# Optimization experiments

Measured on AMD Instinct MI355X. Metric: run time of the kernel, lower is better.

Reference implementation:

```python
import jax, jax.numpy as jnp
from jax import lax
import numpy as np

DN = ('NDHWC', 'DHWIO', 'NDHWC')

def _conv(x, W):
    # stride-1 kernel-3 sparse conv on dense grid: SAME conv; absent voxels are zero
    return lax.conv_general_dilated(x, W, (1, 1, 1), 'SAME', dimension_numbers=DN)

def _tconv(x, W):
    # kernel-2 stride-2 generative transpose conv: exactly doubles each spatial dim
    return lax.conv_transpose(x, W, (2, 2, 2), 'VALID', dimension_numbers=DN)

def _pool(h):
    B, D1, D2, D3, C = h.shape
    return h.reshape(B, D1 // 2, 2, D2 // 2, 2, D3 // 2, 2, C).max(axis=(2, 4, 6))

def _pool_mask(m):
    B, D1, D2, D3 = m.shape
    return m.reshape(B, D1 // 2, 2, D2 // 2, 2, D3 // 2, 2).max(axis=(2, 4, 6))

def _up_mask(m):
    return jnp.repeat(jnp.repeat(jnp.repeat(m, 2, axis=1), 2, axis=2), 2, axis=3)

def setup_inputs() -> dict:
    key = jax.random.key(0)
    ks = jax.random.split(key, 6)
    B, G = 2, 128
    x = jax.random.normal(ks[0], (B, G, G, G, 1), dtype=jnp.float32)
    occ = jax.random.randint(ks[1], (B, G, G, G), 0, 10, dtype=jnp.int32)
    def xavier(k, shape):
        fan_in = np.prod(shape[:-1]); fan_out = shape[-1]
        std = np.sqrt(2.0 / (fan_in + fan_out)).astype(np.float32)
        return jax.random.normal(k, shape, dtype=jnp.float32) * std
    W1 = xavier(ks[2], (3, 3, 3, 1, 16))
    W2 = xavier(ks[3], (3, 3, 3, 16, 4))
    Wt1 = xavier(ks[4], (2, 2, 2, 4, 16))
    Wt2 = xavier(ks[5], (2, 2, 2, 16, 1))
    return {"x": x, "W1": W1, "W2": W2, "Wt1": Wt1, "Wt2": Wt2, "occ": occ}

def reference(x, W1, W2, Wt1, Wt2, occ):
    m0 = (occ == 0).astype(x.dtype)            # occupancy mask at full res
    xm = x * m0[..., None]
    h = jax.nn.relu(_conv(xm, W1)) * m0[..., None]   # coords unchanged
    h = _pool(h); m1 = _pool_mask(m0)                # stride-2 max pool on sparse coords
    h = jax.nn.relu(_conv(h, W2)) * m1[..., None]
    h = _pool(h); m2 = _pool_mask(m1)
    m3 = _up_mask(m2)                                # transpose conv emits all children coords
    h = jax.nn.relu(_tconv(h, Wt1)) * m3[..., None]
    m4 = _up_mask(m3)
    out = jax.nn.sigmoid(_tconv(h, Wt2)) * m4[..., None]
    return out
```

## Files before the change

### kernel.cpp

```cpp
#include <hip/hip_runtime.h>
#include <hip/hip_fp16.h>

#define G 128

typedef _Float16 h2_t __attribute__((ext_vector_type(2)));

union U16 { uint4 u; h2_t h2[4]; };
union HV  { uint4 u; h2_t h2[4]; };
union PK2 { uint2 u; h2_t h[2]; };

__device__ __forceinline__ float dot2f(h2_t a, h2_t b, float c) {
#if __has_builtin(__builtin_amdgcn_fdot2)
    return __builtin_amdgcn_fdot2(a, b, c, false);
#else
    return c + (float)a.x * (float)b.x + (float)a.y * (float)b.y;
#endif
}

__device__ __forceinline__ float dot4(float4 a, float4 b) {
    return a.x * b.x + a.y * b.y + a.z * b.z + a.w * b.w;
}

__global__ __launch_bounds__(256, 1)
void k_conv1_pool(const float* __restrict__ x, const int* __restrict__ occ,
                  const float* __restrict__ W1,
                  __half* __restrict__ h1p, float* __restrict__ m1)
{
    __shared__ __align__(16) _Float16      sx[10 * 18 * 24];
    __shared__ __align__(16) int           pacc[16 * 256];
    __shared__ __align__(4)  unsigned short slist[2048];
    __shared__ __align__(16) h2_t          w1L[216];
    __shared__ __align__(4)  unsigned char sm1[256];
    __shared__ int                         scnt;

    const int bx = blockIdx.x, by = blockIdx.y;
    const int b  = blockIdx.z >> 4, zt = blockIdx.z & 15;
    const int tid = threadIdx.x;

    const int z0 = zt * 8 - 1, y0 = by * 16 - 1;
    const int base_b = b * G * G * G;

    int4   ro[5];
    float4 rx[5];
    #pragma unroll
    for (int it = 0; it < 5; ++it) {
        int c = it * 256 + tid;
        int cc = c < 1080 ? c : 1079;
        int row = cc / 6, seg = cc - row * 6;
        int lz  = row / 18, ly = row - lz * 18;
        int gz = z0 + lz, gy = y0 + ly;
        int gxc = (bx << 4) - 4 + (seg << 2);
        bool inb = (unsigned)gz < 128u && (unsigned)gy < 128u && (unsigned)gxc < 128u;
        int gi = inb ? base_b + (gz * G + gy) * G + gxc : base_b;
        ro[it] = *(const int4*)(occ + gi);
        rx[it] = *(const float4*)(x + gi);
    }

    if (tid == 0) scnt = 0;
    {
        uint4 z4 = make_uint4(0u, 0u, 0u, 0u);
        uint4* p4 = (uint4*)pacc;
        p4[tid] = z4; p4[tid + 256] = z4; p4[tid + 512] = z4; p4[tid + 768] = z4;
    }
    if (tid < 64) ((unsigned*)sm1)[tid] = 0u;
    if (tid < 216) {
        float2 f = ((const float2*)W1)[tid];
        h2_t w; w.x = (_Float16)f.x; w.y = (_Float16)f.y;
        w1L[tid] = w;
    }
    __syncthreads();

    #pragma unroll
    for (int it = 0; it < 5; ++it) {
        int c = it * 256 + tid;
        if (c < 1080) {
            int row = c / 6, seg = c - row * 6;
            int lz  = row / 18, ly = row - lz * 18;
            int gz = z0 + lz, gy = y0 + ly;
            int gxc = (bx << 4) - 4 + (seg << 2);
            bool inb = (unsigned)gz < 128u && (unsigned)gy < 128u && (unsigned)gxc < 128u;
            int4   o4 = ro[it];
            float4 x4 = rx[it];
            if (!inb) o4 = make_int4(1, 1, 1, 1);
            h2_t p01, p23;
            p01.x = (o4.x == 0) ? (_Float16)x4.x : (_Float16)0.f;
            p01.y = (o4.y == 0) ? (_Float16)x4.y : (_Float16)0.f;
            p23.x = (o4.z == 0) ? (_Float16)x4.z : (_Float16)0.f;
            p23.y = (o4.w == 0) ? (_Float16)x4.w : (_Float16)0.f;
            PK2 pk; pk.h[0] = p01; pk.h[1] = p23;
            *(uint2*)&sx[row * 24 + (seg << 2)] = pk.u;

            if ((unsigned)(lz - 1) < 8u && (unsigned)(ly - 1) < 16u &&
                (unsigned)(seg - 1) < 4u) {
                int mb = (o4.x == 0 ? 1 : 0) | (o4.y == 0 ? 2 : 0) |
                         (o4.z == 0 ? 4 : 0) | (o4.w == 0 ? 8 : 0);
                if (mb) {
                    int cnt  = __popc(mb);
                    int base = atomicAdd(&scnt, cnt);
                    int cz = lz - 1, cy = ly - 1, cx0v = (seg << 2) - 4;
                    int cellb = (cz >> 1) * 64 + (cy >> 1) * 8;
                    #pragma unroll
                    for (int j = 0; j < 4; ++j) {
                        if (mb & (1 << j)) {
                            slist[base++] = (unsigned short)((cz << 8) | (cy << 4) | (cx0v + j));
                            sm1[cellb + ((cx0v + j) >> 1)] = (unsigned char)1;
                        }
                    }
                }
            }
        }
    }
    __syncthreads();

    const int n = scnt;

    const h2_t zero = (h2_t)(_Float16)0.f;
    for (int kb = 0; kb < n; kb += 256) {
        const int idx = kb + tid;
        if (idx < n) {
            const int code = slist[idx];
            const int cz = code >> 8, cy = (code >> 4) & 15, cx = code & 15;
            const int sb = ((cz + 1) * 18 + (cy + 1)) * 24 + cx + 4;
            h2_t acc[8];
            #pragma unroll
            for (int c = 0; c < 8; ++c) acc[c] = zero;
            #pragma unroll
            for (int kz = 0; kz < 3; ++kz)
            #pragma unroll
            for (int ky = 0; ky < 3; ++ky)
            #pragma unroll
            for (int kx = 0; kx < 3; ++kx) {
                _Float16 v = sx[sb + (kz - 1) * 432 + (ky - 1) * 24 + (kx - 1)];
                h2_t v2 = {v, v};
                const h2_t* w = &w1L[((kz * 3 + ky) * 3 + kx) * 8];
                #pragma unroll
                for (int c = 0; c < 8; ++c) acc[c] = v2 * w[c] + acc[c];
            }
            const int cell = (cz >> 1) * 64 + (cy >> 1) * 8 + (cx >> 1);
            #pragma unroll
            for (int c = 0; c < 8; ++c) {
                atomicMax(&pacc[(2 * c) * 256 + cell],
                          __float_as_int(fmaxf((float)acc[c].x, 0.f)));
                atomicMax(&pacc[(2 * c + 1) * 256 + cell],
                          __float_as_int(fmaxf((float)acc[c].y, 0.f)));
            }
        }
    }
    __syncthreads();

    const int tx = tid & 7, ty = (tid >> 3) & 7, tz = tid >> 6;
    const int pz = zt * 4 + tz, py = by * 8 + ty, px = bx * 8 + tx;
    const int vidx = ((b * 64 + pz) * 64 + py) * 64 + px;
    HV p0, p1;
    #pragma unroll
    for (int c = 0; c < 4; ++c) {
        h2_t a, bq;
        a.x  = (_Float16)__int_as_float(pacc[(2 * c) * 256 + tid]);
        a.y  = (_Float16)__int_as_float(pacc[(2 * c + 1) * 256 + tid]);
        bq.x = (_Float16)__int_as_float(pacc[(8 + 2 * c) * 256 + tid]);
        bq.y = (_Float16)__int_as_float(pacc[(9 + 2 * c) * 256 + tid]);
        p0.h2[c] = a; p1.h2[c] = bq;
    }
    uint4* o = (uint4*)&h1p[(size_t)vidx * 16];
    o[0] = p0.u;
    o[1] = p1.u;
    m1[vidx] = sm1[tid] ? 1.f : 0.f;
}

__global__ __launch_bounds__(256)
void k_conv2_dec(const __half* __restrict__ h1p, const float* __restrict__ m1,
                 const float* __restrict__ W2,
                 const float* __restrict__ Wt1, const float* __restrict__ Wt2,
                 float* __restrict__ out)
{
    __shared__ uint4  tile[2200];
    __shared__ float4 wt1[128];
    __shared__ float4 wt2[32];
    __shared__ __align__(16) h2_t w2L[864];
    __shared__ float4 sh_h[64];
    __shared__ float  sh_m[64];

    const int bx = blockIdx.x, by = blockIdx.y;
    const int b  = blockIdx.z >> 3, bz = blockIdx.z & 7;
    const int tid = threadIdx.x;

    const int z0 = bz * 8 - 1, y0 = by * 8 - 1, x0 = bx * 8 - 1;

    uint4 ra[5], rb4[5];
    #pragma unroll
    for (int it = 0; it < 5; ++it) {
        int g = it * 256 + tid;
        int gg = g < 1100 ? g : 1099;
        int z = gg / 110, r = gg - z * 110, y = r / 11, xx = r - y * 11;
        int gz = z0 + z, gy = y0 + y, gx = x0 + xx;
        bool inb = (unsigned)gz < 64u && (unsigned)gy < 64u && (unsigned)gx < 64u;
        size_t vi = inb ? (size_t)(((b * 64 + gz) * 64 + gy) * 64 + gx) : 0;
        const uint4* src = (const uint4*)&h1p[vi * 16];
        ra[it]  = src[0];
        rb4[it] = src[1];
    }

    if (tid < 128) wt1[tid] = ((const float4*)Wt1)[tid];
    if (tid < 32)  wt2[tid] = ((const float4*)Wt2)[tid];
    #pragma unroll
    for (int it = 0; it < 4; ++it) {
        int i = it * 256 + tid;
        if (i < 864) {
            int t = i >> 5, rr = i & 31, co = rr >> 3, p = rr & 7;
            h2_t w;
            w.x = (_Float16)W2[t * 64 + (2 * p) * 4 + co];
            w.y = (_Float16)W2[t * 64 + (2 * p + 1) * 4 + co];
            w2L[i] = w;
        }
    }

    #pragma unroll
    for (int it = 0; it < 5; ++it) {
        int g = it * 256 + tid;
        if (g < 1100) {
            int z = g / 110, r = g - z * 110, y = r / 11, xx = r - y * 11;
            int gz = z0 + z, gy = y0 + y, gx = x0 + xx;
            bool inb = (unsigned)gz < 64u && (unsigned)gy < 64u && (unsigned)gx < 64u;
            uint4 a0 = ra[it], a1 = rb4[it];
            if (!inb) { a0 = make_uint4(0u, 0u, 0u, 0u); a1 = a0; }
            tile[g]        = a0;
            tile[1100 + g] = a1;
        }
    }
    __syncthreads();

    const int dy = tid & 1, dz = (tid >> 1) & 1;
    const int qx = (tid >> 2) & 3, Y = (tid >> 4) & 3, Z = (tid >> 6) & 3;
    const int cx0 = 2 * qx, cy = 2 * Y + dy, cz = 2 * Z + dz;

    float acc[2][4] = {{0.f, 0.f, 0.f, 0.f}, {0.f, 0.f, 0.f, 0.f}};

    #pragma unroll
    for (int kz = 0; kz < 3; ++kz)
    #pragma unroll
    for (int ky = 0; ky < 3; ++ky) {
        const int rb = (cz + kz) * 110 + (cy + ky) * 11 + cx0;
        h2_t hp[2][4][4];
        #pragma unroll
        for (int hh = 0; hh < 2; ++hh)
        #pragma unroll
        for (int xi = 0; xi < 4; ++xi) {
            U16 a; a.u = tile[hh * 1100 + rb + xi];
            #pragma unroll
            for (int p = 0; p < 4; ++p) hp[hh][xi][p] = a.h2[p];
        }
        const int t3 = (kz * 3 + ky) * 3;
        #pragma unroll
        for (int kx = 0; kx < 3; ++kx) {
            const h2_t* w = &w2L[(t3 + kx) * 32];
            #pragma unroll
            for (int j = 0; j < 2; ++j) {
                #pragma unroll
                for (int co = 0; co < 4; ++co) {
                    float a = acc[j][co];
                    #pragma unroll
                    for (int hh = 0; hh < 2; ++hh)
                    #pragma unroll
                    for (int p = 0; p < 4; ++p)
                        a = dot2f(hp[hh][kx + j][p], w[co * 8 + 4 * hh + p], a);
                    acc[j][co] = a;
                }
            }
        }
    }

    const int gcz = bz * 8 + cz, gcy = by * 8 + cy, gcx = bx * 8 + cx0;
    const float mv0 = m1[((b * 64 + gcz) * 64 + gcy) * 64 + gcx];
    const float mv1 = m1[((b * 64 + gcz) * 64 + gcy) * 64 + gcx + 1];
    float m = fmaxf(mv0, mv1);
    float r0 = fmaxf(fmaxf(acc[0][0], 0.f) * mv0, fmaxf(acc[1][0], 0.f) * mv1);
    float r1 = fmaxf(fmaxf(acc[0][1], 0.f) * mv0, fmaxf(acc[1][1], 0.f) * mv1);
    float r2 = fmaxf(fmaxf(acc[0][2], 0.f) * mv0, fmaxf(acc[1][2], 0.f) * mv1);
    float r3 = fmaxf(fmaxf(acc[0][3], 0.f) * mv0, fmaxf(acc[1][3], 0.f) * mv1);

    #pragma unroll
    for (int mask = 1; mask <= 2; mask <<= 1) {
        r0 = fmaxf(r0, __shfl_xor(r0, mask));
        r1 = fmaxf(r1, __shfl_xor(r1, mask));
        r2 = fmaxf(r2, __shfl_xor(r2, mask));
        r3 = fmaxf(r3, __shfl_xor(r3, mask));
        m  = fmaxf(m,  __shfl_xor(m,  mask));
    }
    if ((tid & 3) == 0) {
        int p = Z * 16 + Y * 4 + qx;
        sh_h[p] = make_float4(r0, r1, r2, r3);
        sh_m[p] = m;
    }
    __syncthreads();

    {
        const int p  = tid >> 2;
        const int a  = (tid >> 1) & 1;
        const int bb = tid & 1;
        const int pZ = p >> 4, pY = (p >> 2) & 3, pq = p & 3;
        const int pz = bz * 4 + pZ, py = by * 4 + pY, pxq = bx * 4 + pq;

        const float mm = sh_m[p];
        const float4 hv = sh_h[p];

        const int b0q = ((((1 - a) * 2 + (1 - bb)) * 2) + 1) * 16;
        const int b1q = ((((1 - a) * 2 + (1 - bb)) * 2) + 0) * 16;
        float4 t0q[4], t1q[4];
        #pragma unroll
        for (int q = 0; q < 4; ++q) {
            float4 a0 = wt1[b0q + q],      a1 = wt1[b0q + 4 + q];
            float4 a2 = wt1[b0q + 8 + q],  a3 = wt1[b0q + 12 + q];
            float4 c0 = wt1[b1q + q],      c1 = wt1[b1q + 4 + q];
            float4 c2 = wt1[b1q + 8 + q],  c3 = wt1[b1q + 12 + q];
            float4 s0, s1;
            s0.x = hv.x * a0.x + hv.y * a1.x + hv.z * a2.x + hv.w * a3.x;
            s0.y = hv.x * a0.y + hv.y * a1.y + hv.z * a2.y + hv.w * a3.y;
            s0.z = hv.x * a0.z + hv.y * a1.z + hv.z * a2.z + hv.w * a3.z;
            s0.w = hv.x * a0.w + hv.y * a1.w + hv.z * a2.w + hv.w * a3.w;
            s1.x = hv.x * c0.x + hv.y * c1.x + hv.z * c2.x + hv.w * c3.x;
            s1.y = hv.x * c0.y + hv.y * c1.y + hv.z * c2.y + hv.w * c3.y;
            s1.z = hv.x * c0.z + hv.y * c1.z + hv.z * c2.z + hv.w * c3.z;
            s1.w = hv.x * c0.w + hv.y * c1.w + hv.z * c2.w + hv.w * c3.w;
            t0q[q] = make_float4(fmaxf(s0.x, 0.f), fmaxf(s0.y, 0.f),
                                 fmaxf(s0.z, 0.f), fmaxf(s0.w, 0.f));
            t1q[q] = make_float4(fmaxf(s1.x, 0.f), fmaxf(s1.y, 0.f),
                                 fmaxf(s1.z, 0.f), fmaxf(s1.w, 0.f));
        }

        #pragma unroll
        for (int e = 0; e < 2; ++e) {
            #pragma unroll
            for (int f = 0; f < 2; ++f) {
                const int d  = 4 * pz + 2 * a + e;
                const int hh = 4 * py + 2 * bb + f;
                const int be = ((1 - e) * 2 + (1 - f)) * 2;
                const float4* wg0 = &wt2[(be + 1) * 4];
                const float4* wg1 = &wt2[(be + 0) * 4];
                float s00 = dot4(t0q[0], wg0[0]) + dot4(t0q[1], wg0[1])
                          + dot4(t0q[2], wg0[2]) + dot4(t0q[3], wg0[3]);
                float s01 = dot4(t0q[0], wg1[0]) + dot4(t0q[1], wg1[1])
                          + dot4(t0q[2], wg1[2]) + dot4(t0q[3], wg1[3]);
                float s10 = dot4(t1q[0], wg0[0]) + dot4(t1q[1], wg0[1])
                          + dot4(t1q[2], wg0[2]) + dot4(t1q[3], wg0[3]);
                float s11 = dot4(t1q[0], wg1[0]) + dot4(t1q[1], wg1[1])
                          + dot4(t1q[2], wg1[2]) + dot4(t1q[3], wg1[3]);
                float4 o;
                o.x = mm / (1.f + __expf(-s00));
                o.y = mm / (1.f + __expf(-s01));
                o.z = mm / (1.f + __expf(-s10));
                o.w = mm / (1.f + __expf(-s11));
                *(float4*)&out[((b * G + d) * G + hh) * G + 4 * pxq] = o;
            }
        }
    }
}

extern "C" void kernel_launch(void* const* d_in, const int* in_sizes, int n_in,
                              void* d_out, int out_size, void* d_ws, size_t ws_size,
                              hipStream_t stream) {
    (void)in_sizes; (void)n_in; (void)out_size; (void)ws_size;
    const float* x   = (const float*)d_in[0];
    const float* W1  = (const float*)d_in[1];
    const float* W2  = (const float*)d_in[2];
    const float* Wt1 = (const float*)d_in[3];
    const float* Wt2 = (const float*)d_in[4];
    const int*   occ = (const int*)d_in[5];
    float* out = (float*)d_out;

    char* ws = (char*)d_ws;
    __half* h1p = (__half*)ws;
    float*  m1  = (float*)(ws + 8388608ull * sizeof(__half));

    k_conv1_pool<<<dim3(8, 8, 32), dim3(256), 0, stream>>>(x, occ, W1, h1p, m1);
    k_conv2_dec<<<dim3(8, 8, 16), dim3(256), 0, stream>>>(h1p, m1, W2, Wt1, Wt2, out);
}
```

Measured before the change: 146.3 us.

## Compact active voxels per block and skip conv2 on masked-out coordinates

The conv2+decoder kernel now builds a per-block list of voxels whose level-1 mask is set, using ballot and a shared counter, and computes the 3x3x3 conv only for those. Pooling to parents uses shared atomicMax on float bits instead of lane shuffles. Blocks cover half the z-extent, which halves the tile and doubles the grid. This trades the two-voxel x-reuse per thread and adds atomics and an extra sync in exchange for skipping masked work.

```diff
diff --git a/kernel.cpp b/kernel.cpp
--- a/kernel.cpp
+++ b/kernel.cpp
@@ -173,24 +173,26 @@
                  const float* __restrict__ Wt1, const float* __restrict__ Wt2,
                  float* __restrict__ out)
 {
-    __shared__ uint4  tile[2200];
+    __shared__ uint4  tile[1320];
     __shared__ float4 wt1[128];
     __shared__ float4 wt2[32];
     __shared__ __align__(16) h2_t w2L[864];
-    __shared__ float4 sh_h[64];
-    __shared__ float  sh_m[64];
+    __shared__ int    pacc[128];
+    __shared__ int    pm[32];
+    __shared__ unsigned char slist[256];
+    __shared__ int    scnt;
 
     const int bx = blockIdx.x, by = blockIdx.y;
-    const int b  = blockIdx.z >> 3, bz = blockIdx.z & 7;
+    const int b  = blockIdx.z >> 4, bz = blockIdx.z & 15;
     const int tid = threadIdx.x;
 
-    const int z0 = bz * 8 - 1, y0 = by * 8 - 1, x0 = bx * 8 - 1;
-
-    uint4 ra[5], rb4[5];
-    #pragma unroll
-    for (int it = 0; it < 5; ++it) {
+    const int z0 = bz * 4 - 1, y0 = by * 8 - 1, x0 = bx * 8 - 1;
+
+    uint4 ra[3], rb4[3];
+    #pragma unroll
+    for (int it = 0; it < 3; ++it) {
         int g = it * 256 + tid;
-        int gg = g < 1100 ? g : 1099;
+        int gg = g < 660 ? g : 659;
         int z = gg / 110, r = gg - z * 110, y = r / 11, xx = r - y * 11;
         int gz = z0 + z, gy = y0 + y, gx = x0 + xx;
         bool inb = (unsigned)gz < 64u && (unsigned)gy < 64u && (unsigned)gx < 64u;
@@ -200,8 +202,13 @@
         rb4[it] = src[1];
     }
 
-    if (tid < 128) wt1[tid] = ((const float4*)Wt1)[tid];
-    if (tid < 32)  wt2[tid] = ((const float4*)Wt2)[tid];
+    const int cx_ = tid & 7, cy_ = (tid >> 3) & 7, cz_ = tid >> 6;
+    const float mv = m1[((b * 64 + (bz * 4 + cz_)) * 64 + (by * 8 + cy_)) * 64
+                        + (bx * 8 + cx_)];
+
+    if (tid == 0) scnt = 0;
+    if (tid < 128) { wt1[tid] = ((const float4*)Wt1)[tid]; pacc[tid] = 0; }
+    if (tid < 32)  { wt2[tid] = ((const float4*)Wt2)[tid]; pm[tid] = 0; }
     #pragma unroll
     for (int it = 0; it < 4; ++it) {
         int i = it * 256 + tid;
@@ -213,95 +220,94 @@
             w2L[i] = w;
         }
     }
-
-    #pragma unroll
-    for (int it = 0; it < 5; ++it) {
+    __syncthreads();
+
+    #pragma unroll
+    for (int it = 0; it < 3; ++it) {
         int g = it * 256 + tid;
-        if (g < 1100) {
+        if (g < 660) {
             int z = g / 110, r = g - z * 110, y = r / 11, xx = r - y * 11;
             int gz = z0 + z, gy = y0 + y, gx = x0 + xx;
             bool inb = (unsigned)gz < 64u && (unsigned)gy < 64u && (unsigned)gx < 64u;
             uint4 a0 = ra[it], a1 = rb4[it];
             if (!inb) { a0 = make_uint4(0u, 0u, 0u, 0u); a1 = a0; }
-            tile[g]        = a0;
-            tile[1100 + g] = a1;
-        }
-    }
-    __syncthreads();
-
-    const int dy = tid & 1, dz = (tid >> 1) & 1;
-    const int qx = (tid >> 2) & 3, Y = (tid >> 4) & 3, Z = (tid >> 6) & 3;
-    const int cx0 = 2 * qx, cy = 2 * Y + dy, cz = 2 * Z + dz;
-
-    float acc[2][4] = {{0.f, 0.f, 0.f, 0.f}, {0.f, 0.f, 0.f, 0.f}};
-
-    #pragma unroll
-    for (int kz = 0; kz < 3; ++kz)
-    #pragma unroll
-    for (int ky = 0; ky < 3; ++ky) {
-        const int rb = (cz + kz) * 110 + (cy + ky) * 11 + cx0;
-        h2_t hp[2][4][4];
-        #pragma unroll
-        for (int hh = 0; hh < 2; ++hh)
-        #pragma unroll
-        for (int xi = 0; xi < 4; ++xi) {
-            U16 a; a.u = tile[hh * 1100 + rb + xi];
-            #pragma unroll
-            for (int p = 0; p < 4; ++p) hp[hh][xi][p] = a.h2[p];
-        }
-        const int t3 = (kz * 3 + ky) * 3;
-        #pragma unroll
-        for (int kx = 0; kx < 3; ++kx) {
-            const h2_t* w = &w2L[(t3 + kx) * 32];
-            #pragma unroll
-            for (int j = 0; j < 2; ++j) {
+            tile[g]       = a0;
+            tile[660 + g] = a1;
+        }
+    }
+    {
+        const int lane = tid & 63;
+        bool act = (mv != 0.f);
+        unsigned long long bal = __ballot(act);
+        int wtot = __popcll(bal);
+        int wbase = 0;
+        if (lane == 0 && wtot) wbase = atomicAdd(&scnt, wtot);
+        wbase = __shfl(wbase, 0);
+        if (act) {
+            int pre = __popcll(bal & ((1ull << lane) - 1ull));
+            slist[wbase + pre] = (unsigned char)tid;
+            pm[(cz_ >> 1) * 16 + (cy_ >> 1) * 4 + (cx_ >> 1)] = 1;
+        }
+    }
+    __syncthreads();
+
+    const int n = scnt;
+
+    if (tid < n) {
+        const int code = slist[tid];
+        const int cx = code & 7, cy = (code >> 3) & 7, cz = code >> 6;
+        float acc[4] = {0.f, 0.f, 0.f, 0.f};
+        #pragma unroll
+        for (int kz = 0; kz < 3; ++kz)
+        #pragma unroll
+        for (int ky = 0; ky < 3; ++ky) {
+            const int rb = ((cz + kz) * 10 + (cy + ky)) * 11 + cx;
+            h2_t hp[2][3][4];
+            #pragma unroll
+            for (int hh = 0; hh < 2; ++hh)
+            #pragma unroll
+            for (int xi = 0; xi < 3; ++xi) {
+                U16 a; a.u = tile[hh * 660 + rb + xi];
+                #pragma unroll
+                for (int p = 0; p < 4; ++p) hp[hh][xi][p] = a.h2[p];
+            }
+            const int t3 = (kz * 3 + ky) * 3;
+            #pragma unroll
+            for (int kx = 0; kx < 3; ++kx) {
+                const h2_t* w = &w2L[(t3 + kx) * 32];
                 #pragma unroll
                 for (int co = 0; co < 4; ++co) {
-                    float a = acc[j][co];
+                    float a = acc[co];
                     #pragma unroll
                     for (int hh = 0; hh < 2; ++hh)
                     #pragma unroll
                     for (int p = 0; p < 4; ++p)
-                        a = dot2f(hp[hh][kx + j][p], w[co * 8 + 4 * hh + p], a);
-                    acc[j][co] = a;
+                        a = dot2f(hp[hh][kx][p], w[co * 8 + 4 * hh + p], a);
+                    acc[co] = a;
                 }
             }
         }
-    }
-
-    const int gcz = bz * 8 + cz, gcy = by * 8 + cy, gcx = bx * 8 + cx0;
-    const float mv0 = m1[((b * 64 + gcz) * 64 + gcy) * 64 + gcx];
-    const float mv1 = m1[((b * 64 + gcz) * 64 + gcy) * 64 + gcx + 1];
-    float m = fmaxf(mv0, mv1);
-    float r0 = fmaxf(fmaxf(acc[0][0], 0.f) * mv0, fmaxf(acc[1][0], 0.f) * mv1);
-    float r1 = fmaxf(fmaxf(acc[0][1], 0.f) * mv0, fmaxf(acc[1][1], 0.f) * mv1);
-    float r2 = fmaxf(fmaxf(acc[0][2], 0.f) * mv0, fmaxf(acc[1][2], 0.f) * mv1);
-    float r3 = fmaxf(fmaxf(acc[0][3], 0.f) * mv0, fmaxf(acc[1][3], 0.f) * mv1);
-
-    #pragma unroll
-    for (int mask = 1; mask <= 2; mask <<= 1) {
-        r0 = fmaxf(r0, __shfl_xor(r0, mask));
-        r1 = fmaxf(r1, __shfl_xor(r1, mask));
-        r2 = fmaxf(r2, __shfl_xor(r2, mask));
-        r3 = fmaxf(r3, __shfl_xor(r3, mask));
-        m  = fmaxf(m,  __shfl_xor(m,  mask));
-    }
-    if ((tid & 3) == 0) {
-        int p = Z * 16 + Y * 4 + qx;
-        sh_h[p] = make_float4(r0, r1, r2, r3);
-        sh_m[p] = m;
+        const int parent = (cz >> 1) * 16 + (cy >> 1) * 4 + (cx >> 1);
+        #pragma unroll
+        for (int co = 0; co < 4; ++co)
+            atomicMax(&pacc[co * 32 + parent],
+                      __float_as_int(fmaxf(acc[co], 0.f)));
     }
     __syncthreads();
 
     {
-        const int p  = tid >> 2;
-        const int a  = (tid >> 1) & 1;
-        const int bb = tid & 1;
+        const int p  = tid >> 3;
+        const int a  = (tid >> 2) & 1;
+        const int bb = (tid >> 1) & 1;
+        const int e  = tid & 1;
         const int pZ = p >> 4, pY = (p >> 2) & 3, pq = p & 3;
-        const int pz = bz * 4 + pZ, py = by * 4 + pY, pxq = bx * 4 + pq;
-
-        const float mm = sh_m[p];
-        const float4 hv = sh_h[p];
+        const int pz = bz * 2 + pZ, py = by * 4 + pY, pxq = bx * 4 + pq;
+
+        const float mm = pm[p] ? 1.f : 0.f;
+        const float4 hv = make_float4(__int_as_float(pacc[p]),
+                                      __int_as_float(pacc[32 + p]),
+                                      __int_as_float(pacc[64 + p]),
+                                      __int_as_float(pacc[96 + p]));
 
         const int b0q = ((((1 - a) * 2 + (1 - bb)) * 2) + 1) * 16;
         const int b1q = ((((1 - a) * 2 + (1 - bb)) * 2) + 0) * 16;
@@ -327,30 +333,27 @@
                                  fmaxf(s1.z, 0.f), fmaxf(s1.w, 0.f));
         }
 
-        #pragma unroll
-        for (int e = 0; e < 2; ++e) {
-            #pragma unroll
-            for (int f = 0; f < 2; ++f) {
-                const int d  = 4 * pz + 2 * a + e;
-                const int hh = 4 * py + 2 * bb + f;
-                const int be = ((1 - e) * 2 + (1 - f)) * 2;
-                const float4* wg0 = &wt2[(be + 1) * 4];
-                const float4* wg1 = &wt2[(be + 0) * 4];
-                float s00 = dot4(t0q[0], wg0[0]) + dot4(t0q[1], wg0[1])
-                          + dot4(t0q[2], wg0[2]) + dot4(t0q[3], wg0[3]);
-                float s01 = dot4(t0q[0], wg1[0]) + dot4(t0q[1], wg1[1])
-                          + dot4(t0q[2], wg1[2]) + dot4(t0q[3], wg1[3]);
-                float s10 = dot4(t1q[0], wg0[0]) + dot4(t1q[1], wg0[1])
-                          + dot4(t1q[2], wg0[2]) + dot4(t1q[3], wg0[3]);
-                float s11 = dot4(t1q[0], wg1[0]) + dot4(t1q[1], wg1[1])
-                          + dot4(t1q[2], wg1[2]) + dot4(t1q[3], wg1[3]);
-                float4 o;
-                o.x = mm / (1.f + __expf(-s00));
-                o.y = mm / (1.f + __expf(-s01));
-                o.z = mm / (1.f + __expf(-s10));
-                o.w = mm / (1.f + __expf(-s11));
-                *(float4*)&out[((b * G + d) * G + hh) * G + 4 * pxq] = o;
-            }
+        const int d = 4 * pz + 2 * a + e;
+        #pragma unroll
+        for (int f = 0; f < 2; ++f) {
+            const int hh = 4 * py + 2 * bb + f;
+            const int be = ((1 - e) * 2 + (1 - f)) * 2;
+            const float4* wg0 = &wt2[(be + 1) * 4];
+            const float4* wg1 = &wt2[(be + 0) * 4];
+            float s00 = dot4(t0q[0], wg0[0]) + dot4(t0q[1], wg0[1])
+                      + dot4(t0q[2], wg0[2]) + dot4(t0q[3], wg0[3]);
+            float s01 = dot4(t0q[0], wg1[0]) + dot4(t0q[1], wg1[1])
+                      + dot4(t0q[2], wg1[2]) + dot4(t0q[3], wg1[3]);
+            float s10 = dot4(t1q[0], wg0[0]) + dot4(t1q[1], wg0[1])
+                      + dot4(t1q[2], wg0[2]) + dot4(t1q[3], wg0[3]);
+            float s11 = dot4(t1q[0], wg1[0]) + dot4(t1q[1], wg1[1])
+                      + dot4(t1q[2], wg1[2]) + dot4(t1q[3], wg1[3]);
+            float4 o;
+            o.x = mm / (1.f + __expf(-s00));
+            o.y = mm / (1.f + __expf(-s01));
+            o.z = mm / (1.f + __expf(-s10));
+            o.w = mm / (1.f + __expf(-s11));
+            *(float4*)&out[((b * G + d) * G + hh) * G + 4 * pxq] = o;
         }
     }
 }
@@ -372,5 +375,5 @@
     float*  m1  = (float*)(ws + 8388608ull * sizeof(__half));
 
     k_conv1_pool<<<dim3(8, 8, 32), dim3(256), 0, stream>>>(x, occ, W1, h1p, m1);
-    k_conv2_dec<<<dim3(8, 8, 16), dim3(256), 0, stream>>>(h1p, m1, W2, Wt1, Wt2, out);
-}
+    k_conv2_dec<<<dim3(8, 8, 32), dim3(256), 0, stream>>>(h1p, m1, W2, Wt1, Wt2, out);
+}
```

Result: slower. 152.5 us (+4.2%).

## Precompute fp16 W2 in conv1 kernel and halve conv2 LDS tile via channel-half passes

Applied to the files above, without the earlier changes.

The W2 fp16 repacking moves out of every conv2 block into a single block of the conv1 kernel, which writes it to workspace; conv2 then reads the weights from global memory instead of LDS. The conv2 input tile is cut to one 8-channel half, processed in two passes with a barrier between them. This halves tile LDS and removes the w2L array to raise occupancy. The cost is extra barriers, the loss of overlap between prefetch and compute, and weights now fetched through global/scalar loads inside the inner loop.

```diff
diff --git a/kernel.cpp b/kernel.cpp
--- a/kernel.cpp
+++ b/kernel.cpp
@@ -23,8 +23,9 @@
 
 __global__ __launch_bounds__(256, 1)
 void k_conv1_pool(const float* __restrict__ x, const int* __restrict__ occ,
-                  const float* __restrict__ W1,
-                  __half* __restrict__ h1p, float* __restrict__ m1)
+                  const float* __restrict__ W1, const float* __restrict__ W2,
+                  __half* __restrict__ h1p, float* __restrict__ m1,
+                  __half* __restrict__ w2h)
 {
     __shared__ __align__(16) _Float16      sx[10 * 18 * 24];
     __shared__ __align__(16) int           pacc[16 * 256];
@@ -54,6 +55,18 @@
         int gi = inb ? base_b + (gz * G + gy) * G + gxc : base_b;
         ro[it] = *(const int4*)(occ + gi);
         rx[it] = *(const float4*)(x + gi);
+    }
+
+    if (bx == 0 && by == 0 && blockIdx.z == 0) {
+        #pragma unroll
+        for (int it = 0; it < 4; ++it) {
+            int i = it * 256 + tid;
+            if (i < 864) {
+                int t = i >> 5, rr = i & 31, co = rr >> 3, p = rr & 7;
+                w2h[2 * i]     = __float2half(W2[t * 64 + (2 * p) * 4 + co]);
+                w2h[2 * i + 1] = __float2half(W2[t * 64 + (2 * p + 1) * 4 + co]);
+            }
+        }
     }
 
     if (tid == 0) scnt = 0;
@@ -169,14 +182,13 @@
 
 __global__ __launch_bounds__(256)
 void k_conv2_dec(const __half* __restrict__ h1p, const float* __restrict__ m1,
-                 const float* __restrict__ W2,
+                 const h2_t* __restrict__ w2h,
                  const float* __restrict__ Wt1, const float* __restrict__ Wt2,
                  float* __restrict__ out)
 {
-    __shared__ uint4  tile[2200];
+    __shared__ uint4  tile[1100];
     __shared__ float4 wt1[128];
     __shared__ float4 wt2[32];
-    __shared__ __align__(16) h2_t w2L[864];
     __shared__ float4 sh_h[64];
     __shared__ float  sh_m[64];
 
@@ -184,50 +196,10 @@
     const int b  = blockIdx.z >> 3, bz = blockIdx.z & 7;
     const int tid = threadIdx.x;
 
-    const int z0 = bz * 8 - 1, y0 = by * 8 - 1, x0 = bx * 8 - 1;
-
-    uint4 ra[5], rb4[5];
-    #pragma unroll
-    for (int it = 0; it < 5; ++it) {
-        int g = it * 256 + tid;
-        int gg = g < 1100 ? g : 1099;
-        int z = gg / 110, r = gg - z * 110, y = r / 11, xx = r - y * 11;
-        int gz = z0 + z, gy = y0 + y, gx = x0 + xx;
-        bool inb = (unsigned)gz < 64u && (unsigned)gy < 64u && (unsigned)gx < 64u;
-        size_t vi = inb ? (size_t)(((b * 64 + gz) * 64 + gy) * 64 + gx) : 0;
-        const uint4* src = (const uint4*)&h1p[vi * 16];
-        ra[it]  = src[0];
-        rb4[it] = src[1];
-    }
-
     if (tid < 128) wt1[tid] = ((const float4*)Wt1)[tid];
     if (tid < 32)  wt2[tid] = ((const float4*)Wt2)[tid];
-    #pragma unroll
-    for (int it = 0; it < 4; ++it) {
-        int i = it * 256 + tid;
-        if (i < 864) {
-            int t = i >> 5, rr = i & 31, co = rr >> 3, p = rr & 7;
-            h2_t w;
-            w.x = (_Float16)W2[t * 64 + (2 * p) * 4 + co];
-            w.y = (_Float16)W2[t * 64 + (2 * p + 1) * 4 + co];
-            w2L[i] = w;
-        }
-    }
-
-    #pragma unroll
-    for (int it = 0; it < 5; ++it) {
-        int g = it * 256 + tid;
-        if (g < 1100) {
-            int z = g / 110, r = g - z * 110, y = r / 11, xx = r - y * 11;
-            int gz = z0 + z, gy = y0 + y, gx = x0 + xx;
-            bool inb = (unsigned)gz < 64u && (unsigned)gy < 64u && (unsigned)gx < 64u;
-            uint4 a0 = ra[it], a1 = rb4[it];
-            if (!inb) { a0 = make_uint4(0u, 0u, 0u, 0u); a1 = a0; }
-            tile[g]        = a0;
-            tile[1100 + g] = a1;
-        }
-    }
-    __syncthreads();
+
+    const int z0 = bz * 8 - 1, y0 = by * 8 - 1, x0 = bx * 8 - 1;
 
     const int dy = tid & 1, dz = (tid >> 1) & 1;
     const int qx = (tid >> 2) & 3, Y = (tid >> 4) & 3, Z = (tid >> 6) & 3;
@@ -235,35 +207,48 @@
 
     float acc[2][4] = {{0.f, 0.f, 0.f, 0.f}, {0.f, 0.f, 0.f, 0.f}};
 
-    #pragma unroll
-    for (int kz = 0; kz < 3; ++kz)
-    #pragma unroll
-    for (int ky = 0; ky < 3; ++ky) {
-        const int rb = (cz + kz) * 110 + (cy + ky) * 11 + cx0;
-        h2_t hp[2][4][4];
-        #pragma unroll
-        for (int hh = 0; hh < 2; ++hh)
-        #pragma unroll
-        for (int xi = 0; xi < 4; ++xi) {
-            U16 a; a.u = tile[hh * 1100 + rb + xi];
-            #pragma unroll
-            for (int p = 0; p < 4; ++p) hp[hh][xi][p] = a.h2[p];
-        }
-        const int t3 = (kz * 3 + ky) * 3;
-        #pragma unroll
-        for (int kx = 0; kx < 3; ++kx) {
-            const h2_t* w = &w2L[(t3 + kx) * 32];
-            #pragma unroll
-            for (int j = 0; j < 2; ++j) {
+    for (int h = 0; h < 2; ++h) {
+        if (h) __syncthreads();
+        #pragma unroll
+        for (int it = 0; it < 5; ++it) {
+            int g = it * 256 + tid;
+            if (g < 1100) {
+                int z = g / 110, r = g - z * 110, y = r / 11, xx = r - y * 11;
+                int gz = z0 + z, gy = y0 + y, gx = x0 + xx;
+                uint4 a = make_uint4(0u, 0u, 0u, 0u);
+                if ((unsigned)gz < 64u && (unsigned)gy < 64u && (unsigned)gx < 64u)
+                    a = ((const uint4*)&h1p[(size_t)(((b * 64 + gz) * 64 + gy) * 64 + gx) * 16])[h];
+                tile[g] = a;
+            }
+        }
+        __syncthreads();
+
+        #pragma unroll
+        for (int kz = 0; kz < 3; ++kz)
+        #pragma unroll
+        for (int ky = 0; ky < 3; ++ky) {
+            const int rb = (cz + kz) * 110 + (cy + ky) * 11 + cx0;
+            h2_t hp[4][4];
+            #pragma unroll
+            for (int xi = 0; xi < 4; ++xi) {
+                U16 a; a.u = tile[rb + xi];
                 #pragma unroll
-                for (int co = 0; co < 4; ++co) {
-                    float a = acc[j][co];
+                for (int p = 0; p < 4; ++p) hp[xi][p] = a.h2[p];
+            }
+            const int t3 = (kz * 3 + ky) * 3;
+            #pragma unroll
+            for (int kx = 0; kx < 3; ++kx) {
+                const h2_t* w = w2h + (t3 + kx) * 32 + 4 * h;
+                #pragma unroll
+                for (int j = 0; j < 2; ++j) {
                     #pragma unroll
-                    for (int hh = 0; hh < 2; ++hh)
-                    #pragma unroll
-                    for (int p = 0; p < 4; ++p)
-                        a = dot2f(hp[hh][kx + j][p], w[co * 8 + 4 * hh + p], a);
-                    acc[j][co] = a;
+                    for (int co = 0; co < 4; ++co) {
+                        float a = acc[j][co];
+                        #pragma unroll
+                        for (int p = 0; p < 4; ++p)
+                            a = dot2f(hp[kx + j][p], w[co * 8 + p], a);
+                        acc[j][co] = a;
+                    }
                 }
             }
         }
@@ -370,7 +355,8 @@
     char* ws = (char*)d_ws;
     __half* h1p = (__half*)ws;
     float*  m1  = (float*)(ws + 8388608ull * sizeof(__half));
-
-    k_conv1_pool<<<dim3(8, 8, 32), dim3(256), 0, stream>>>(x, occ, W1, h1p, m1);
-    k_conv2_dec<<<dim3(8, 8, 16), dim3(256), 0, stream>>>(h1p, m1, W2, Wt1, Wt2, out);
-}
+    __half* w2h = (__half*)(m1 + 524288);
+
+    k_conv1_pool<<<dim3(8, 8, 32), dim3(256), 0, stream>>>(x, occ, W1, W2, h1p, m1, w2h);
+    k_conv2_dec<<<dim3(8, 8, 16), dim3(256), 0, stream>>>(h1p, m1, (const h2_t*)w2h, Wt1, Wt2, out);
+}
```

After: 147.2 us. Within noise of the previous version (+0.6%).
